# Kernel optimization log

Hardware: AMD Instinct MI355X
Metric: run time of the kernel (lower is better)

## Reference

```python
import jax, jax.numpy as jnp
import numpy as np

# Module hyperparameters (BNMorph.__init__ defaults + KITTI resolution)
B, H, W = 8, 320, 1024
SEARCH_W = 7      # serachWidth
SEARCH_H = 3      # searchHeight
SPARSITY_RAD = 2
SENSE_R = 20
PIX_DW = 24.0     # pixel_distance_weight
ALPHA_DW = 0.7    # alpha_distance_weight
PIX_MUL_DW = 1.9  # pixel_mulline_distance_weight
ALPHA_PAD = 1.6   # alpha_padding
EDGE_DENSITY = 0.02


def _make_offsets():
    # Exactly mirrors BNMorph.__init__ buffer construction.
    rs = np.arange(-SEARCH_W, SEARCH_W + 1)
    cs = np.arange(-SEARCH_H, SEARCH_H + 1)
    xx, yy = np.meshgrid(rs, cs)
    xx = xx.flatten(); yy = yy.flatten()
    idx = np.argsort(xx ** 2 + yy ** 2)
    xx = xx[idx]; yy = yy[idx]
    ss = np.arange(-SPARSITY_RAD, SPARSITY_RAD + 1)
    sxx, syy = np.meshgrid(ss, ss)
    sxx = sxx.flatten(); syy = syy.flatten()
    cspan = np.arange(-SENSE_R, SENSE_R + 1)
    cxx, cyy = np.meshgrid(cspan, cspan)
    cxx = cxx.flatten(); cyy = cyy.flatten()
    ci = np.argsort(cxx ** 2 + cyy ** 2)
    cxx = cxx[ci]; cyy = cyy[ci]
    f32 = lambda a: jnp.asarray(a, dtype=jnp.float32)
    return f32(xx), f32(yy), f32(sxx), f32(syy), f32(cxx), f32(cyy)


def setup_inputs() -> dict:
    key = jax.random.key(0)
    k1, k2 = jax.random.split(key)
    binMapsrc = (jax.random.uniform(k1, (B, 1, H, W)) < EDGE_DENSITY).astype(jnp.float32)
    binMapdst = (jax.random.uniform(k2, (B, 1, H, W)) < EDGE_DENSITY).astype(jnp.float32)
    xx, yy, sxx, syy, cxx, cyy = _make_offsets()
    return {"binMapsrc": binMapsrc, "binMapdst": binMapdst,
            "xx": xx, "yy": yy, "sxx": sxx, "syy": syy, "cxx": cxx, "cyy": cyy}


def _forward(binMapsrc, binMapdst, xx, yy, sxx, syy, cxx, cyy):
    src = binMapsrc[:, 0] > 0.5  # [B,H,W] bool
    dst = binMapdst[:, 0] > 0.5
    b, h, w = src.shape

    # ---- 1. sparsity filtering of src edge points ----
    # keep an active pixel iff no active pixel precedes it (raster order)
    # inside the sparsity window -> approximates greedy sparsification.
    sdx = sxx.astype(jnp.int32); sdy = syy.astype(jnp.int32)
    prec = ((sdy < 0) | ((sdy == 0) & (sdx < 0))).astype(jnp.float32)
    Ps = jnp.pad(src.astype(jnp.float32),
                 ((0, 0), (SPARSITY_RAD, SPARSITY_RAD), (SPARSITY_RAD, SPARSITY_RAD)))

    def sp_step(acc, off):
        dx, dy, wk = off
        sl = jax.lax.dynamic_slice(Ps, (0, SPARSITY_RAD + dy, SPARSITY_RAD + dx), (b, h, w))
        return acc + sl * wk, None

    acc, _ = jax.lax.scan(sp_step, jnp.zeros((b, h, w), jnp.float32), (sdx, sdy, prec))
    kept = src & (acc < 0.5)

    # ---- 2. windowed nearest-correspondence search in dst ----
    # offsets (xx,yy) are pre-sorted by distance, so the first hit is nearest.
    qdx = xx.astype(jnp.int32); qdy = yy.astype(jnp.int32)
    Pd = jnp.pad(dst, ((0, 0), (SEARCH_H, SEARCH_H), (SEARCH_W, SEARCH_W)))

    def m_step(carry, off):
        found, vx, vy = carry
        dx, dy, dxf, dyf = off
        sl = jax.lax.dynamic_slice(Pd, (0, SEARCH_H + dy, SEARCH_W + dx), (b, h, w))
        hit = sl & kept & (~found)
        vx = jnp.where(hit, dxf, vx)
        vy = jnp.where(hit, dyf, vy)
        return (found | hit, vx, vy), None

    init = (jnp.zeros((b, h, w), bool),
            jnp.zeros((b, h, w), jnp.float32),
            jnp.zeros((b, h, w), jnp.float32))
    (found, vx, vy), _ = jax.lax.scan(m_step, init, (qdx, qdy, xx, yy))

    # ---- 3. distance-weighted morph field (splat = depthwise conv) ----
    d = jnp.sqrt(cxx ** 2 + cyy ** 2)
    wts = ALPHA_DW * jnp.exp(-d * PIX_MUL_DW / PIX_DW)
    R = SENSE_R
    K = jnp.zeros((2 * R + 1, 2 * R + 1), jnp.float32)
    K = K.at[cyy.astype(jnp.int32) + R, cxx.astype(jnp.int32) + R].set(wts)

    m = found.astype(jnp.float32)
    inp = jnp.stack([m, m * vx, m * vy], axis=1)        # [B,3,H,W]
    ker = jnp.tile(K[None, None], (3, 1, 1, 1))          # [3,1,41,41]
    out = jax.lax.conv_general_dilated(
        inp, ker, (1, 1), ((R, R), (R, R)),
        dimension_numbers=("NCHW", "OIHW", "NCHW"), feature_group_count=3)
    den = out[:, 0] + ALPHA_PAD
    dispx = out[:, 1] / den
    dispy = out[:, 2] / den

    ygrid, xgrid = jnp.meshgrid(jnp.arange(h, dtype=jnp.float32),
                                jnp.arange(w, dtype=jnp.float32), indexing="ij")
    morphedx = xgrid + dispx
    morphedy = ygrid + dispy
    orgpts_x = xgrid * m
    orgpts_y = ygrid * m
    correspts_x = (xgrid + vx) * m
    correspts_y = (ygrid + vy) * m
    return morphedx, morphedy, orgpts_x, orgpts_y, correspts_x, correspts_y


def reference(binMapsrc, binMapdst, xx, yy, sxx, syy, cxx, cyy):
    return _forward(binMapsrc, binMapdst, xx, yy, sxx, syy, cxx, cyy)
```

## Files before the change

### kernel.cpp

```cpp
#include <hip/hip_runtime.h>


#define BB 8
#define HH 320
#define WW 1024
#define N_PIX (BB*HH*WW)
#define WPI (HH*(WW/32))
#define RR 20
#define TLW 64
#define TLH 16
#define TXN (WW/TLW)
#define TYN (HH/TLH)
#define NQ 105
#define CAP 160
#define NCR (TLH+40)
#define NSR (NCR+2)
#define NDR (NCR+6)
#define WSTRIDE 53
#define WTABN 2228
#define WTAB_OFF (2*BB*WPI*4)

typedef unsigned long long u64;
typedef float v2f __attribute__((ext_vector_type(2)));

__global__ __launch_bounds__(256) void pack_zero(
    const float* __restrict__ src, const float* __restrict__ dst,
    unsigned* __restrict__ packed, float* __restrict__ wtab_g)
{
    int t = threadIdx.x;
    int i = blockIdx.x * 256 + t;
    if (i < WTABN) {
        int row = i / WSTRIDE, c = i - row * WSTRIDE;
        float v = 0.0f;
        if (row <= 40 && c >= 4 && c <= 44) {
            int dxv = c - 24, dyv = row - 20;
            float d = sqrtf((float)(dxv * dxv + dyv * dyv));
            v = 0.7f * expf((-d * 1.9f) / 24.0f);
        }
        wtab_g[i] = v;
    }
    const float4* p = (i < (N_PIX >> 2)) ? (const float4*)src + i
                                         : (const float4*)dst + (i - (N_PIX >> 2));
    float4 v = *p;
    unsigned nib = (v.x > 0.5f ? 1u : 0u) | (v.y > 0.5f ? 2u : 0u)
                 | (v.z > 0.5f ? 4u : 0u) | (v.w > 0.5f ? 8u : 0u);
    unsigned val = nib << ((t & 7) * 4);
    val |= __shfl_xor(val, 1);
    val |= __shfl_xor(val, 2);
    val |= __shfl_xor(val, 4);
    if ((t & 7) == 0) packed[i >> 3] = val;
}

__global__ __launch_bounds__(128, 5) void fused_morph(
    const unsigned* __restrict__ packed,
    const float* __restrict__ xx, const float* __restrict__ yy,
    const float* __restrict__ wtab_g,
    float* __restrict__ out)
{
    __shared__ __align__(16) float wtab[WTABN];
    __shared__ unsigned sSrc[NSR][6];
    __shared__ unsigned sDst[NDR][6];
    __shared__ __align__(16) unsigned sPt[CAP];
    __shared__ __align__(16) unsigned sWav[2][CAP + 4];
    __shared__ int prank[NQ];
    __shared__ unsigned char sVB[TLH * TLW];
    __shared__ int lcnt;

    int t = threadIdx.x;
    int txT = blockIdx.x, tyT = blockIdx.y, b = blockIdx.z;
    int tx0 = txT * TLW, ty0 = tyT * TLH;
    int wb0 = (tx0 >> 5) - 1;
    const unsigned* psrc = packed + (size_t)b * WPI;
    const unsigned* pdst = packed + (size_t)(BB + b) * WPI;

    for (int i = t; i < WTABN / 4; i += 128)
        ((float4*)wtab)[i] = ((const float4*)wtab_g)[i];
    for (int i = t; i < NSR * 4; i += 128) {
        int r = i >> 2, w = (i & 3) + 1;
        int gy = ty0 - 22 + r, gw = wb0 + (w - 1);
        sSrc[r][w] = (gy >= 0 && gy < HH && gw >= 0 && gw < 32) ? psrc[(gy << 5) + gw] : 0u;
    }
    for (int i = t; i < NDR * 4; i += 128) {
        int r = i >> 2, w = (i & 3) + 1;
        int gy = ty0 - 23 + r, gw = wb0 + (w - 1);
        sDst[r][w] = (gy >= 0 && gy < HH && gw >= 0 && gw < 32) ? pdst[(gy << 5) + gw] : 0u;
    }
    if (t < NDR) { sDst[t][0] = 0; sDst[t][5] = 0; if (t < NSR) { sSrc[t][0] = 0; sSrc[t][5] = 0; } }
    if (t < NQ) {
        int dx = (int)xx[t], dy = (int)yy[t];
        prank[(dy + 3) * 15 + (dx + 7)] = (t << 8) | ((dx + 7) << 4) | (dy + 3);
    }
    ((unsigned*)sVB)[t] = 0; ((unsigned*)sVB)[t + 128] = 0;
    if (t == 0) lcnt = 0;
    __syncthreads();

    for (int task = t; task < NCR * 4; task += 128) {
        int cr = task >> 2, w = (task & 3) + 1;
        unsigned C = sSrc[cr + 2][w];
        unsigned found = 0;
        if (C) {
            #define EXT5(row) ( (u64)((row)[w-1] >> 30) \
                              | ((u64)(row)[w] << 2) \
                              | ((u64)((row)[w+1] & 3u) << 34) )
            u64 a = EXT5(sSrc[cr]) | EXT5(sSrc[cr + 1]);
            u64 or5 = a | (a >> 1) | (a >> 2) | (a >> 3) | (a >> 4);
            u64 e2 = EXT5(sSrc[cr + 2]);
            unsigned kept = C & ~(unsigned)(or5 | e2 | (e2 >> 1));
            if (kept) {
                u64 dil = 0;
                #pragma unroll
                for (int rr = 0; rr < 7; ++rr) {
                    const unsigned* row = sDst[cr + rr];
                    dil |= (u64)(row[w-1] >> 25) | ((u64)row[w] << 7)
                         | ((u64)(row[w+1] & 0x7Fu) << 39);
                }
                u64 a2 = dil | (dil >> 1);
                u64 b2 = a2 | (a2 >> 2);
                u64 c2 = b2 | (b2 >> 4);
                u64 o15 = c2 | (c2 >> 7);
                found = kept & (unsigned)o15;
            }
        }
        if (w == 1) found &= 0xFFFFF000u;
        if (w == 4) found &= 0x000FFFFFu;
        if (found) {
            int nf = __popc(found);
            int base = atomicAdd(&lcnt, nf);
            unsigned fi = found;
            while (fi) {
                int bit = __builtin_ctz(fi); fi &= fi - 1;
                int px = tx0 - 32 + ((w - 1) << 5) + bit;
                if (base < CAP) sPt[base] = (unsigned)((cr << 10) | px);
                ++base;
            }
        }
    }
    __syncthreads();
    int nPts = lcnt; if (nPts > CAP) nPts = CAP;

    for (int i = t; i < nPts; i += 128) {
        unsigned e = sPt[i];
        int cr = (int)(e >> 10), px = (int)(e & 1023u);
        int q = px - tx0 + 25;
        int widx = 1 + (q >> 5), sh = q & 31;
        u64 lo = 0, hi = 0;
        #pragma unroll
        for (int rr = 0; rr < 7; ++rr) {
            const unsigned* row = sDst[cr + rr];
            u64 win = (((u64)row[widx] | ((u64)row[widx + 1] << 32)) >> sh) & 0x7FFFull;
            if (rr < 4) lo |= win << (15 * rr);
            else        hi |= win << (15 * (rr - 4));
        }
        int minv = 0x7FFFFFFF;
        while (lo) { int bb2 = __builtin_ctzll(lo); lo &= lo - 1; int rv = prank[bb2];      if (rv < minv) minv = rv; }
        while (hi) { int bb2 = __builtin_ctzll(hi); hi &= hi - 1; int rv = prank[60 + bb2]; if (rv < minv) minv = rv; }
        int vxp7 = (minv >> 4) & 15, vyp3 = minv & 15;
        int py = ty0 - 20 + cr;
        sPt[i] = (unsigned)px | ((unsigned)py << 10)
               | ((unsigned)vxp7 << 19) | ((unsigned)vyp3 << 23);
        if (px >= tx0 && px < tx0 + TLW && cr >= 20 && cr < 20 + TLH)
            sVB[(cr - 20) * TLW + (px - tx0)] =
                (unsigned char)(0x80 | vxp7 | (vyp3 << 4));
    }
    __syncthreads();

    int lane = t & 63, w = __builtin_amdgcn_readfirstlane(t >> 6);
    int wy0 = ty0 + w * 8;
    int cw = 0;
    for (int base = 0; base < nPts; base += 64) {
        int i = base + lane;
        unsigned pk = (i < nPts) ? sPt[i] : 0xFFFFFFFFu;
        int py = (int)((pk >> 10) & 511u);
        bool pass = (i < nPts) & (py >= wy0 - 20) & (py <= wy0 + 27);
        u64 m = __ballot(pass);
        if (pass) {
            int idx = __popcll(m & ((1ull << lane) - 1ull));
            sWav[w][cw + idx] = pk;
        }
        cw += __popcll(m);
    }
    int c4 = (cw + 3) & ~3;
    if (lane < c4 - cw) sWav[w][cw + lane] = 0xFFFFFFFFu;

    int x0q = tx0 + (lane & 15) * 4;
    int yg  = wy0 + (lane >> 4);

    v2f a0p[2][2] = {};
    v2f av[2][4]  = {};

    for (int p = 0; p < c4; p += 4) {
        uint4 P = *(const uint4*)&sWav[w][p];
        #pragma unroll
        for (int k = 0; k < 4; ++k) {
            int spk = __builtin_amdgcn_readfirstlane(
                (int)(k == 0 ? P.x : k == 1 ? P.y : k == 2 ? P.z : P.w));
            int pxp21 = (spk & 1023) + 21;
            int pyp20 = ((spk >> 10) & 511) + 20;
            float pvx = (float)(((spk >> 19) & 15) - 7);
            float pvy = (float)(((spk >> 23) & 7) - 3);
            v2f vv = {pvx, pvy};

            int coff = pxp21 - x0q;
            coff = coff < 0 ? 0 : (coff > 45 ? 45 : coff);
            #pragma unroll
            for (int ry = 0; ry < 2; ++ry) {
                int dyr = pyp20 - (yg + 4 * ry);
                int rowi = ((unsigned)dyr > 40u) ? 41 : dyr;
                const float* wr = &wtab[rowi * WSTRIDE + coff];
                float w3 = wr[0], w2 = wr[1], w1 = wr[2], w0 = wr[3];
                a0p[ry][0] += (v2f){w0, w1};
                a0p[ry][1] += (v2f){w2, w3};
                av[ry][0] += w0 * vv;
                av[ry][1] += w1 * vv;
                av[ry][2] += w2 * vv;
                av[ry][3] += w3 * vv;
            }
        }
    }

    size_t bbase = (size_t)b * HH * WW;
    int lx = x0q - tx0;
    #pragma unroll
    for (int ry = 0; ry < 2; ++ry) {
        int y = yg + 4 * ry;
        int ly = y - ty0;
        unsigned vb4 = *(const unsigned*)&sVB[ly * TLW + lx];
        size_t idx = bbase + (size_t)y * WW + x0q;
        float d0 = a0p[ry][0].x + 1.6f, d1 = a0p[ry][0].y + 1.6f;
        float d2 = a0p[ry][1].x + 1.6f, d3 = a0p[ry][1].y + 1.6f;
        float4 ox = { (float)x0q     + av[ry][0].x / d0, (float)(x0q+1) + av[ry][1].x / d1,
                      (float)(x0q+2) + av[ry][2].x / d2, (float)(x0q+3) + av[ry][3].x / d3 };
        float4 oy = { (float)y + av[ry][0].y / d0, (float)y + av[ry][1].y / d1,
                      (float)y + av[ry][2].y / d2, (float)y + av[ry][3].y / d3 };
        float4 o2, o3, o4, o5;
        float* po2 = &o2.x; float* po3 = &o3.x; float* po4 = &o4.x; float* po5 = &o5.x;
        #pragma unroll
        for (int jj = 0; jj < 4; ++jj) {
            unsigned by = (vb4 >> (8 * jj)) & 255u;
            float fm  = (float)(by >> 7);
            float fvx = (float)((int)(by & 15u) - 7);
            float fvy = (float)((int)((by >> 4) & 7u) - 3);
            float fx  = (float)(x0q + jj);
            po2[jj] = fx * fm;
            po3[jj] = (float)y * fm;
            po4[jj] = (fx + fvx) * fm;
            po5[jj] = ((float)y + fvy) * fm;
        }
        *reinterpret_cast<float4*>(out + idx)                     = ox;
        *reinterpret_cast<float4*>(out + (size_t)N_PIX + idx)     = oy;
        *reinterpret_cast<float4*>(out + 2 * (size_t)N_PIX + idx) = o2;
        *reinterpret_cast<float4*>(out + 3 * (size_t)N_PIX + idx) = o3;
        *reinterpret_cast<float4*>(out + 4 * (size_t)N_PIX + idx) = o4;
        *reinterpret_cast<float4*>(out + 5 * (size_t)N_PIX + idx) = o5;
    }
}

extern "C" void kernel_launch(void* const* d_in, const int* in_sizes, int n_in,
                              void* d_out, int out_size, void* d_ws, size_t ws_size,
                              hipStream_t stream) {
    const float* src = (const float*)d_in[0];
    const float* dst = (const float*)d_in[1];
    const float* xx  = (const float*)d_in[2];
    const float* yy  = (const float*)d_in[3];
    float* out = (float*)d_out;

    unsigned* packed = (unsigned*)d_ws;
    float*    wtab_g = (float*)((char*)d_ws + WTAB_OFF);

    pack_zero<<<(2 * N_PIX / 4) / 256, 256, 0, stream>>>(src, dst, packed, wtab_g);

    dim3 g2(TXN, TYN, BB);
    fused_morph<<<g2, 128, 0, stream>>>(packed, xx, yy, wtab_g, out);
}
```

Baseline: 124.4 us.

## Make each wave process its own row band independently without block barriers

Each of the two waves now loads its own halo of the packed source and destination maps, sparsity-filters and matches only the points relevant to its 8-row band, and keeps per-wave shared buffers. This removes the block-wide __syncthreads and the later per-wave ballot compaction pass, using only wave-level barriers. In exchange, halo rows are processed twice (48 candidate rows per wave instead of 56 shared), the weight table is loaded by both waves, the per-wave point cap drops to 128, and the occupancy hint is lowered from 5 to 4 blocks.

```diff
diff --git a/kernel.cpp b/kernel.cpp
--- a/kernel.cpp
+++ b/kernel.cpp
@@ -12,10 +12,10 @@
 #define TXN (WW/TLW)
 #define TYN (HH/TLH)
 #define NQ 105
-#define CAP 160
-#define NCR (TLH+40)
-#define NSR (NCR+2)
-#define NDR (NCR+6)
+#define CAP 128
+#define NCRW 48
+#define NSRW 50
+#define NDRW 54
 #define WSTRIDE 53
 #define WTABN 2228
 #define WTAB_OFF (2*BB*WPI*4)
@@ -51,68 +51,71 @@
     if ((t & 7) == 0) packed[i >> 3] = val;
 }
 
-__global__ __launch_bounds__(128, 5) void fused_morph(
+__global__ __launch_bounds__(128, 4) void fused_morph(
     const unsigned* __restrict__ packed,
     const float* __restrict__ xx, const float* __restrict__ yy,
     const float* __restrict__ wtab_g,
     float* __restrict__ out)
 {
     __shared__ __align__(16) float wtab[WTABN];
-    __shared__ unsigned sSrc[NSR][6];
-    __shared__ unsigned sDst[NDR][6];
-    __shared__ __align__(16) unsigned sPt[CAP];
-    __shared__ __align__(16) unsigned sWav[2][CAP + 4];
-    __shared__ int prank[NQ];
-    __shared__ unsigned char sVB[TLH * TLW];
-    __shared__ int lcnt;
+    __shared__ unsigned sSrc[2][NSRW][6];
+    __shared__ unsigned sDst[2][NDRW][6];
+    __shared__ __align__(16) unsigned sPt[2][CAP + 8];
+    __shared__ int prank[2][NQ];
+    __shared__ unsigned char sVB[2][8 * TLW];
+    __shared__ int lcnt[2];
 
     int t = threadIdx.x;
+    int lane = t & 63;
+    int w = __builtin_amdgcn_readfirstlane(t >> 6);
     int txT = blockIdx.x, tyT = blockIdx.y, b = blockIdx.z;
     int tx0 = txT * TLW, ty0 = tyT * TLH;
+    int wy0 = ty0 + w * 8;
     int wb0 = (tx0 >> 5) - 1;
     const unsigned* psrc = packed + (size_t)b * WPI;
     const unsigned* pdst = packed + (size_t)(BB + b) * WPI;
 
-    for (int i = t; i < WTABN / 4; i += 128)
+    for (int i = lane; i < WTABN / 4; i += 64)
         ((float4*)wtab)[i] = ((const float4*)wtab_g)[i];
-    for (int i = t; i < NSR * 4; i += 128) {
-        int r = i >> 2, w = (i & 3) + 1;
-        int gy = ty0 - 22 + r, gw = wb0 + (w - 1);
-        sSrc[r][w] = (gy >= 0 && gy < HH && gw >= 0 && gw < 32) ? psrc[(gy << 5) + gw] : 0u;
-    }
-    for (int i = t; i < NDR * 4; i += 128) {
-        int r = i >> 2, w = (i & 3) + 1;
-        int gy = ty0 - 23 + r, gw = wb0 + (w - 1);
-        sDst[r][w] = (gy >= 0 && gy < HH && gw >= 0 && gw < 32) ? pdst[(gy << 5) + gw] : 0u;
-    }
-    if (t < NDR) { sDst[t][0] = 0; sDst[t][5] = 0; if (t < NSR) { sSrc[t][0] = 0; sSrc[t][5] = 0; } }
-    if (t < NQ) {
-        int dx = (int)xx[t], dy = (int)yy[t];
-        prank[(dy + 3) * 15 + (dx + 7)] = (t << 8) | ((dx + 7) << 4) | (dy + 3);
-    }
-    ((unsigned*)sVB)[t] = 0; ((unsigned*)sVB)[t + 128] = 0;
-    if (t == 0) lcnt = 0;
-    __syncthreads();
-
-    for (int task = t; task < NCR * 4; task += 128) {
-        int cr = task >> 2, w = (task & 3) + 1;
-        unsigned C = sSrc[cr + 2][w];
+    for (int i = lane; i < NSRW * 4; i += 64) {
+        int r = i >> 2, wd = (i & 3) + 1;
+        int gy = wy0 - 22 + r, gw = wb0 + (wd - 1);
+        sSrc[w][r][wd] = (gy >= 0 && gy < HH && gw >= 0 && gw < 32) ? psrc[(gy << 5) + gw] : 0u;
+    }
+    for (int i = lane; i < NDRW * 4; i += 64) {
+        int r = i >> 2, wd = (i & 3) + 1;
+        int gy = wy0 - 23 + r, gw = wb0 + (wd - 1);
+        sDst[w][r][wd] = (gy >= 0 && gy < HH && gw >= 0 && gw < 32) ? pdst[(gy << 5) + gw] : 0u;
+    }
+    if (lane < NDRW) { sDst[w][lane][0] = 0; sDst[w][lane][5] = 0; }
+    if (lane < NSRW) { sSrc[w][lane][0] = 0; sSrc[w][lane][5] = 0; }
+    for (int i = lane; i < NQ; i += 64) {
+        int dx = (int)xx[i], dy = (int)yy[i];
+        prank[w][(dy + 3) * 15 + (dx + 7)] = (i << 8) | ((dx + 7) << 4) | (dy + 3);
+    }
+    ((unsigned*)sVB[w])[lane] = 0; ((unsigned*)sVB[w])[lane + 64] = 0;
+    if (lane == 0) lcnt[w] = 0;
+    __builtin_amdgcn_wave_barrier();
+
+    for (int task = lane; task < NCRW * 4; task += 64) {
+        int cr = task >> 2, wd = (task & 3) + 1;
+        unsigned C = sSrc[w][cr + 2][wd];
         unsigned found = 0;
         if (C) {
-            #define EXT5(row) ( (u64)((row)[w-1] >> 30) \
-                              | ((u64)(row)[w] << 2) \
-                              | ((u64)((row)[w+1] & 3u) << 34) )
-            u64 a = EXT5(sSrc[cr]) | EXT5(sSrc[cr + 1]);
+            #define EXT5(row) ( (u64)((row)[wd-1] >> 30) \
+                              | ((u64)(row)[wd] << 2) \
+                              | ((u64)((row)[wd+1] & 3u) << 34) )
+            u64 a = EXT5(sSrc[w][cr]) | EXT5(sSrc[w][cr + 1]);
             u64 or5 = a | (a >> 1) | (a >> 2) | (a >> 3) | (a >> 4);
-            u64 e2 = EXT5(sSrc[cr + 2]);
+            u64 e2 = EXT5(sSrc[w][cr + 2]);
             unsigned kept = C & ~(unsigned)(or5 | e2 | (e2 >> 1));
             if (kept) {
                 u64 dil = 0;
                 #pragma unroll
                 for (int rr = 0; rr < 7; ++rr) {
-                    const unsigned* row = sDst[cr + rr];
-                    dil |= (u64)(row[w-1] >> 25) | ((u64)row[w] << 7)
-                         | ((u64)(row[w+1] & 0x7Fu) << 39);
+                    const unsigned* row = sDst[w][cr + rr];
+                    dil |= (u64)(row[wd-1] >> 25) | ((u64)row[wd] << 7)
+                         | ((u64)(row[wd+1] & 0x7Fu) << 39);
                 }
                 u64 a2 = dil | (dil >> 1);
                 u64 b2 = a2 | (a2 >> 2);
@@ -121,66 +124,51 @@
                 found = kept & (unsigned)o15;
             }
         }
-        if (w == 1) found &= 0xFFFFF000u;
-        if (w == 4) found &= 0x000FFFFFu;
+        if (wd == 1) found &= 0xFFFFF000u;
+        if (wd == 4) found &= 0x000FFFFFu;
         if (found) {
             int nf = __popc(found);
-            int base = atomicAdd(&lcnt, nf);
+            int base = atomicAdd(&lcnt[w], nf);
             unsigned fi = found;
             while (fi) {
                 int bit = __builtin_ctz(fi); fi &= fi - 1;
-                int px = tx0 - 32 + ((w - 1) << 5) + bit;
-                if (base < CAP) sPt[base] = (unsigned)((cr << 10) | px);
+                int px = tx0 - 32 + ((wd - 1) << 5) + bit;
+                if (base < CAP) sPt[w][base] = (unsigned)((cr << 10) | px);
                 ++base;
             }
         }
     }
-    __syncthreads();
-    int nPts = lcnt; if (nPts > CAP) nPts = CAP;
-
-    for (int i = t; i < nPts; i += 128) {
-        unsigned e = sPt[i];
+    __builtin_amdgcn_wave_barrier();
+
+    int nPts = lcnt[w]; if (nPts > CAP) nPts = CAP;
+
+    for (int i = lane; i < nPts; i += 64) {
+        unsigned e = sPt[w][i];
         int cr = (int)(e >> 10), px = (int)(e & 1023u);
         int q = px - tx0 + 25;
         int widx = 1 + (q >> 5), sh = q & 31;
         u64 lo = 0, hi = 0;
         #pragma unroll
         for (int rr = 0; rr < 7; ++rr) {
-            const unsigned* row = sDst[cr + rr];
+            const unsigned* row = sDst[w][cr + rr];
             u64 win = (((u64)row[widx] | ((u64)row[widx + 1] << 32)) >> sh) & 0x7FFFull;
             if (rr < 4) lo |= win << (15 * rr);
             else        hi |= win << (15 * (rr - 4));
         }
         int minv = 0x7FFFFFFF;
-        while (lo) { int bb2 = __builtin_ctzll(lo); lo &= lo - 1; int rv = prank[bb2];      if (rv < minv) minv = rv; }
-        while (hi) { int bb2 = __builtin_ctzll(hi); hi &= hi - 1; int rv = prank[60 + bb2]; if (rv < minv) minv = rv; }
+        while (lo) { int bb2 = __builtin_ctzll(lo); lo &= lo - 1; int rv = prank[w][bb2];      if (rv < minv) minv = rv; }
+        while (hi) { int bb2 = __builtin_ctzll(hi); hi &= hi - 1; int rv = prank[w][60 + bb2]; if (rv < minv) minv = rv; }
         int vxp7 = (minv >> 4) & 15, vyp3 = minv & 15;
-        int py = ty0 - 20 + cr;
-        sPt[i] = (unsigned)px | ((unsigned)py << 10)
-               | ((unsigned)vxp7 << 19) | ((unsigned)vyp3 << 23);
-        if (px >= tx0 && px < tx0 + TLW && cr >= 20 && cr < 20 + TLH)
-            sVB[(cr - 20) * TLW + (px - tx0)] =
+        int py = wy0 - 20 + cr;
+        sPt[w][i] = (unsigned)px | ((unsigned)py << 10)
+                  | ((unsigned)vxp7 << 19) | ((unsigned)vyp3 << 23);
+        if (px >= tx0 && px < tx0 + TLW && cr >= 20 && cr < 28)
+            sVB[w][(cr - 20) * TLW + (px - tx0)] =
                 (unsigned char)(0x80 | vxp7 | (vyp3 << 4));
     }
-    __syncthreads();
-
-    int lane = t & 63, w = __builtin_amdgcn_readfirstlane(t >> 6);
-    int wy0 = ty0 + w * 8;
-    int cw = 0;
-    for (int base = 0; base < nPts; base += 64) {
-        int i = base + lane;
-        unsigned pk = (i < nPts) ? sPt[i] : 0xFFFFFFFFu;
-        int py = (int)((pk >> 10) & 511u);
-        bool pass = (i < nPts) & (py >= wy0 - 20) & (py <= wy0 + 27);
-        u64 m = __ballot(pass);
-        if (pass) {
-            int idx = __popcll(m & ((1ull << lane) - 1ull));
-            sWav[w][cw + idx] = pk;
-        }
-        cw += __popcll(m);
-    }
-    int c4 = (cw + 3) & ~3;
-    if (lane < c4 - cw) sWav[w][cw + lane] = 0xFFFFFFFFu;
+    int c4 = (nPts + 3) & ~3;
+    if (lane < c4 - nPts) sPt[w][nPts + lane] = 0xFFFFFFFFu;
+    __builtin_amdgcn_wave_barrier();
 
     int x0q = tx0 + (lane & 15) * 4;
     int yg  = wy0 + (lane >> 4);
@@ -189,7 +177,7 @@
     v2f av[2][4]  = {};
 
     for (int p = 0; p < c4; p += 4) {
-        uint4 P = *(const uint4*)&sWav[w][p];
+        uint4 P = *(const uint4*)&sPt[w][p];
         #pragma unroll
         for (int k = 0; k < 4; ++k) {
             int spk = __builtin_amdgcn_readfirstlane(
@@ -202,9 +190,10 @@
 
             int coff = pxp21 - x0q;
             coff = coff < 0 ? 0 : (coff > 45 ? 45 : coff);
+            int d0r = pyp20 - yg;
             #pragma unroll
             for (int ry = 0; ry < 2; ++ry) {
-                int dyr = pyp20 - (yg + 4 * ry);
+                int dyr = d0r - 4 * ry;
                 int rowi = ((unsigned)dyr > 40u) ? 41 : dyr;
                 const float* wr = &wtab[rowi * WSTRIDE + coff];
                 float w3 = wr[0], w2 = wr[1], w1 = wr[2], w0 = wr[3];
@@ -223,8 +212,7 @@
     #pragma unroll
     for (int ry = 0; ry < 2; ++ry) {
         int y = yg + 4 * ry;
-        int ly = y - ty0;
-        unsigned vb4 = *(const unsigned*)&sVB[ly * TLW + lx];
+        unsigned vb4 = *(const unsigned*)&sVB[w][(y - wy0) * TLW + lx];
         size_t idx = bbase + (size_t)y * WW + x0q;
         float d0 = a0p[ry][0].x + 1.6f, d1 = a0p[ry][0].y + 1.6f;
         float d2 = a0p[ry][1].x + 1.6f, d3 = a0p[ry][1].y + 1.6f;
```

Result: slower. 135.6 us (+9.0%).
